# Performance work log

Hardware: AMD Instinct MI355X
Metric: run time of the kernel (lower is better)

## Reference

```python
import jax, jax.numpy as jnp
import numpy as np

B, T, C, H = 2, 2048, 1024, 16
D = C // H
THETA = 10000.0


def setup_inputs() -> dict:
    key = jax.random.key(0)
    k1, k2, k3 = jax.random.split(key, 3)
    x = jax.random.normal(k1, (B, T, C), dtype=jnp.float32)
    tok_mask = jnp.ones((B, T), dtype=bool)
    # torch Linear weights stored transposed: y = x @ W.T; we store [in, out]
    W_qkv = jax.random.normal(k2, (C, 3 * C), dtype=jnp.float32) / np.sqrt(C)
    W_o = jax.random.normal(k3, (C, C), dtype=jnp.float32) / np.sqrt(C)
    return {"x": x, "tok_mask": tok_mask, "W_qkv": W_qkv, "W_o": W_o}


def _rope_tables(t_len):
    # NOTE: source uses exponents arange(1, D+1, 2)/D and positions starting at 1
    exps = jnp.arange(1, D + 1, 2, dtype=jnp.float32)[: D // 2] / D
    w = 1.0 / (THETA ** exps)                      # [D/2]
    t = jnp.arange(1, t_len + 1, dtype=jnp.float32)  # [T]
    ang = t[:, None] * w[None, :]                  # [T, D/2]
    return jnp.sin(ang), jnp.cos(ang)


def _rope(x, sin, cos):
    # x: [B, H, T, D]; rotate interleaved pairs
    x1 = x[..., ::2]
    x2 = x[..., 1::2]
    r1 = x1 * cos - x2 * sin
    r2 = x1 * sin + x2 * cos
    return jnp.stack((r1, r2), axis=-1).reshape(x.shape)


def reference(x, tok_mask, W_qkv, W_o):
    b, t, c = x.shape
    qkv = x @ W_qkv                                   # [B,T,3C]
    q, k, v = jnp.split(qkv, 3, axis=-1)
    def heads(z):
        return z.reshape(b, t, H, D).transpose(0, 2, 1, 3)  # [B,H,T,D]
    q, k, v = heads(q), heads(k), heads(v)
    sin, cos = _rope_tables(t)
    q = _rope(q, sin, cos)
    k = _rope(k, sin, cos)
    scores = jnp.einsum('bhqd,bhkd->bhqk', q, k) / jnp.sqrt(jnp.float32(D))
    # mask[b,i,j] = tok_mask[b,i] & tok_mask[b,j] & causal
    mask = tok_mask[:, None, :, None] & tok_mask[:, None, None, :]  # [B,1,T,T]
    causal = jnp.tril(jnp.ones((t, t), dtype=bool))
    mask = mask & causal[None, None, :, :]
    scores = jnp.where(mask, scores, jnp.float32(-1e9))
    att = jax.nn.softmax(scores, axis=-1)             # dropout p=0 (eval)
    y = jnp.einsum('bhqk,bhkd->bhqd', att, v)
    y = y.transpose(0, 2, 1, 3).reshape(b, t, c)
    return y @ W_o
```

## Files before the change

### kernel.cpp

```cpp
#include <hip/hip_runtime.h>
#include <hip/hip_bf16.h>

typedef __bf16 bf16x8 __attribute__((ext_vector_type(8)));
typedef short s16x4 __attribute__((ext_vector_type(4)));
typedef float floatx4 __attribute__((ext_vector_type(4)));
typedef __hip_bfloat16 bf16;

#define T_SEQ 2048
#define NH 16
#define HD 64
#define CDIM 1024

__device__ __forceinline__ void gload16(const bf16* g, bf16* ldsbase) {
  __builtin_amdgcn_global_load_lds((const __attribute__((address_space(1))) void*)g,
                                   (__attribute__((address_space(3))) void*)ldsbase, 16, 0, 0);
}

__global__ __launch_bounds__(256) void cast_bf16_kernel(const float* __restrict__ in,
                                                        bf16* __restrict__ out) {
  int i = blockIdx.x * 256 + threadIdx.x;
  const float4 v = ((const float4*)in)[i];
  union { bf16 h[4]; uint2 u; } p;
  p.h[0] = __float2bfloat16(v.x);
  p.h[1] = __float2bfloat16(v.y);
  p.h[2] = __float2bfloat16(v.z);
  p.h[3] = __float2bfloat16(v.w);
  ((uint2*)out)[i] = p.u;
}

__global__ __launch_bounds__(256) void transpose_cast(const float* __restrict__ in,
                                                      bf16* __restrict__ out,
                                                      int R, int Cc) {
  __shared__ float tile[32][33];
  const int bx = blockIdx.x * 32;
  const int by = blockIdx.y * 32;
  const int tx = threadIdx.x & 31, ty = threadIdx.x >> 5;
#pragma unroll
  for (int i = 0; i < 32; i += 8)
    tile[ty + i][tx] = in[(size_t)(by + ty + i) * Cc + bx + tx];
  __syncthreads();
#pragma unroll
  for (int i = 0; i < 32; i += 8)
    out[(size_t)(bx + ty + i) * R + by + tx] = __float2bfloat16(tile[tx][ty + i]);
}

__global__ void rope_tab_kernel(float2* __restrict__ tab) {
  int idx = blockIdx.x * 256 + threadIdx.x;
  int t = idx >> 5, j = idx & 31;
  float w = exp2f(-13.287712379549449f * (float)(2 * j + 1) * (1.0f / 64.0f));
  float ang = (float)(t + 1) * w;
  tab[idx] = make_float2(cosf(ang), sinf(ang));
}

template <int MODE>
__global__ __launch_bounds__(256) void gemm_bt(
    const bf16* __restrict__ A, const bf16* __restrict__ BT, float* __restrict__ CoutF,
    const float2* __restrict__ tab, bf16* __restrict__ Qr, bf16* __restrict__ Kr,
    bf16* __restrict__ Vt, int M, int N, int K) {
  constexpr int LDK = 32;
  __shared__ __align__(16) bf16 As[128 * LDK];
  __shared__ __align__(16) bf16 Bs[128 * LDK];
  const int tid = threadIdx.x, lane = tid & 63, wave = tid >> 6;
  const int quad = lane >> 4, c16 = lane & 15;
  const int tile_m = blockIdx.y * 128, tile_n = blockIdx.x * 128;
  const int wm = (wave >> 1) * 64, wn = (wave & 1) * 64;
  const int r0 = tid >> 2, cp4 = tid & 3;
  bf16* ldsA0 = &As[wave * 512];
  bf16* ldsA1 = &As[2048 + wave * 512];
  bf16* ldsB0 = &Bs[wave * 512];
  bf16* ldsB1 = &Bs[2048 + wave * 512];
  floatx4 acc[4][4] = {};
  for (int k0 = 0; k0 < K; k0 += 32) {
    __syncthreads();
    gload16(&A[(size_t)(tile_m + r0) * K + k0 + cp4 * 8], ldsA0);
    gload16(&A[(size_t)(tile_m + r0 + 64) * K + k0 + cp4 * 8], ldsA1);
    gload16(&BT[(size_t)(tile_n + r0) * K + k0 + cp4 * 8], ldsB0);
    gload16(&BT[(size_t)(tile_n + r0 + 64) * K + k0 + cp4 * 8], ldsB1);
    __syncthreads();
    bf16x8 af[4], bfr[4];
#pragma unroll
    for (int i = 0; i < 4; i++)
      af[i] = *(const bf16x8*)&As[(wm + i * 16 + c16) * LDK + quad * 8];
#pragma unroll
    for (int i = 0; i < 4; i++)
      bfr[i] = *(const bf16x8*)&Bs[(wn + i * 16 + c16) * LDK + quad * 8];
#pragma unroll
    for (int mi = 0; mi < 4; mi++)
#pragma unroll
      for (int ni = 0; ni < 4; ni++)
        acc[mi][ni] = __builtin_amdgcn_mfma_f32_16x16x32_bf16(af[mi], bfr[ni], acc[mi][ni], 0, 0, 0);
  }
  if (MODE == 0) {
#pragma unroll
    for (int mi = 0; mi < 4; mi++) {
      int row0 = tile_m + wm + mi * 16 + quad * 4;
#pragma unroll
      for (int ni = 0; ni < 4; ni++) {
        int col = tile_n + wn + ni * 16 + c16;
#pragma unroll
        for (int r = 0; r < 4; r++)
          CoutF[(size_t)(row0 + r) * N + col] = acc[mi][ni][r];
      }
    }
  } else {
#pragma unroll
    for (int ni = 0; ni < 4; ni++) {
      int colg = tile_n + wn + ni * 16 + c16;
      int seg = colg >> 10;
      int cc = colg & 1023;
      int h = cc >> 6, d = cc & 63, j = d >> 1;
#pragma unroll
      for (int mi = 0; mi < 4; mi++) {
        int row0 = tile_m + wm + mi * 16 + quad * 4;
#pragma unroll
        for (int r = 0; r < 4; r++) {
          int rowg = row0 + r;
          int b = rowg >> 11, t = rowg & 2047;
          float val = acc[mi][ni][r];
          float partner = __shfl_xor(val, 1, 64);
          size_t bh = (size_t)(b * NH + h);
          if (seg == 2) {
            Vt[(bh * HD + d) * T_SEQ + t] = __float2bfloat16(val);
          } else {
            float2 sc = tab[t * 32 + j];
            float outv = ((d & 1) == 0) ? (val * sc.x - partner * sc.y)
                                        : (val * sc.x + partner * sc.y);
            bf16* dst = (seg == 0) ? Qr : Kr;
            dst[(bh * T_SEQ + t) * HD + d] = __float2bfloat16(outv);
          }
        }
      }
    }
  }
}

__global__ __launch_bounds__(256) void attn_kernel(const bf16* __restrict__ Qr,
                                                   const bf16* __restrict__ Kr,
                                                   const bf16* __restrict__ Vt,
                                                   bf16* __restrict__ Y) {
  constexpr int DPAD = 72;
  __shared__ __align__(16) bf16 Ks[64 * DPAD];
  __shared__ __align__(16) bf16 Vs[64 * DPAD];
  __shared__ __align__(16) bf16 Ps[4][16 * DPAD];
  const int qtile = 31 - (blockIdx.x >> 5), bh = blockIdx.x & 31;
  const int b = bh >> 4, h = bh & 15;
  const int tid = threadIdx.x, lane = tid & 63, wave = tid >> 6;
  const int quad = lane >> 4, c16 = lane & 15;
  const size_t hoff = (size_t)bh * T_SEQ * HD;
  const int row0 = tid >> 3, cp = tid & 7;
  const int qbase = qtile * 64;
  const int qg = qbase + wave * 16 + c16;
  bf16x8 qf0 = *(const bf16x8*)&Qr[hoff + (size_t)qg * HD + quad * 8];
  bf16x8 qf1 = *(const bf16x8*)&Qr[hoff + (size_t)qg * HD + 32 + quad * 8];
  floatx4 o_acc[4] = {};
  float m_run = -1e30f, l_run = 0.f;
  bf16x8 kreg0 = *(const bf16x8*)&Kr[hoff + (size_t)row0 * HD + cp * 8];
  bf16x8 kreg1 = *(const bf16x8*)&Kr[hoff + (size_t)(row0 + 32) * HD + cp * 8];
  bf16x8 vreg0 = *(const bf16x8*)&Vt[hoff + (size_t)row0 * T_SEQ + cp * 8];
  bf16x8 vreg1 = *(const bf16x8*)&Vt[hoff + (size_t)(row0 + 32) * T_SEQ + cp * 8];
  for (int kt = 0; kt <= qtile; ++kt) {
    const int kbase = kt * 64;
    __syncthreads();
    *(bf16x8*)&Ks[row0 * DPAD + cp * 8] = kreg0;
    *(bf16x8*)&Ks[(row0 + 32) * DPAD + cp * 8] = kreg1;
    *(bf16x8*)&Vs[row0 * DPAD + cp * 8] = vreg0;
    *(bf16x8*)&Vs[(row0 + 32) * DPAD + cp * 8] = vreg1;
    __syncthreads();
    if (kt < qtile) {
      const int nb = kbase + 64;
      kreg0 = *(const bf16x8*)&Kr[hoff + (size_t)(nb + row0) * HD + cp * 8];
      kreg1 = *(const bf16x8*)&Kr[hoff + (size_t)(nb + row0 + 32) * HD + cp * 8];
      vreg0 = *(const bf16x8*)&Vt[hoff + (size_t)row0 * T_SEQ + nb + cp * 8];
      vreg1 = *(const bf16x8*)&Vt[hoff + (size_t)(row0 + 32) * T_SEQ + nb + cp * 8];
    }
    floatx4 s[4];
#pragma unroll
    for (int nt = 0; nt < 4; nt++) {
      bf16x8 kf0 = *(const bf16x8*)&Ks[(nt * 16 + c16) * DPAD + quad * 8];
      bf16x8 kf1 = *(const bf16x8*)&Ks[(nt * 16 + c16) * DPAD + 32 + quad * 8];
      floatx4 z = {0.f, 0.f, 0.f, 0.f};
      z = __builtin_amdgcn_mfma_f32_16x16x32_bf16(kf0, qf0, z, 0, 0, 0);
      z = __builtin_amdgcn_mfma_f32_16x16x32_bf16(kf1, qf1, z, 0, 0, 0);
      s[nt] = z;
    }
    const bool diag = (kt == qtile);
    float mloc = -1e30f;
#pragma unroll
    for (int nt = 0; nt < 4; nt++)
#pragma unroll
      for (int r = 0; r < 4; r++) {
        float v = s[nt][r] * 0.125f;
        if (diag) {
          int kg = kbase + nt * 16 + quad * 4 + r;
          v = (kg <= qg) ? v : -1e30f;
        }
        s[nt][r] = v;
        mloc = fmaxf(mloc, v);
      }
    mloc = fmaxf(mloc, __shfl_xor(mloc, 16, 64));
    mloc = fmaxf(mloc, __shfl_xor(mloc, 32, 64));
    float mn = fmaxf(m_run, mloc);
    float alpha = __expf(m_run - mn);
    m_run = mn;
    float lloc = 0.f;
    union { bf16 h[4]; s16x4 sv; } ph[4];
#pragma unroll
    for (int nt = 0; nt < 4; nt++)
#pragma unroll
      for (int r = 0; r < 4; r++) {
        float pp = __expf(s[nt][r] - mn);
        lloc += pp;
        ph[nt].h[r] = __float2bfloat16(pp);
      }
    lloc += __shfl_xor(lloc, 16, 64);
    lloc += __shfl_xor(lloc, 32, 64);
    l_run = l_run * alpha + lloc;
#pragma unroll
    for (int nt = 0; nt < 4; nt++)
      *(s16x4*)&Ps[wave][c16 * DPAD + nt * 16 + quad * 4] = ph[nt].sv;
    float a_bc[4];
#pragma unroll
    for (int r = 0; r < 4; r++) a_bc[r] = __shfl(alpha, quad * 4 + r, 16);
#pragma unroll
    for (int dt = 0; dt < 4; dt++)
#pragma unroll
      for (int r = 0; r < 4; r++) o_acc[dt][r] *= a_bc[r];
    bf16x8 pf0 = *(const bf16x8*)&Ps[wave][c16 * DPAD + quad * 8];
    bf16x8 pf1 = *(const bf16x8*)&Ps[wave][c16 * DPAD + 32 + quad * 8];
#pragma unroll
    for (int dt = 0; dt < 4; dt++) {
      bf16x8 vf0 = *(const bf16x8*)&Vs[(dt * 16 + c16) * DPAD + quad * 8];
      bf16x8 vf1 = *(const bf16x8*)&Vs[(dt * 16 + c16) * DPAD + 32 + quad * 8];
      o_acc[dt] = __builtin_amdgcn_mfma_f32_16x16x32_bf16(pf0, vf0, o_acc[dt], 0, 0, 0);
      o_acc[dt] = __builtin_amdgcn_mfma_f32_16x16x32_bf16(pf1, vf1, o_acc[dt], 0, 0, 0);
    }
  }
  float linv = 1.0f / l_run;
  float l_bc[4];
#pragma unroll
  for (int r = 0; r < 4; r++) l_bc[r] = __shfl(linv, quad * 4 + r, 16);
#pragma unroll
  for (int dt = 0; dt < 4; dt++)
#pragma unroll
    for (int r = 0; r < 4; r++) {
      int t = qbase + wave * 16 + quad * 4 + r;
      Y[((size_t)(b * T_SEQ + t)) * CDIM + h * HD + dt * 16 + c16] =
          __float2bfloat16(o_acc[dt][r] * l_bc[r]);
    }
}

extern "C" void kernel_launch(void* const* d_in, const int* in_sizes, int n_in,
                              void* d_out, int out_size, void* d_ws, size_t ws_size,
                              hipStream_t stream) {
  const float* x    = (const float*)d_in[0];
  const float* Wqkv = (const float*)d_in[2];
  const float* Wo   = (const float*)d_in[3];
  float* out = (float*)d_out;

  bf16* ws    = (bf16*)d_ws;
  bf16* Xb    = ws;
  bf16* WqkvT = Xb + 4194304;
  bf16* WoT   = WqkvT + 3072 * 1024;
  bf16* Qr    = WoT + 1024 * 1024;
  bf16* Kr    = Qr + 4194304;
  bf16* Vt    = Kr + 4194304;
  bf16* Y     = Vt + 4194304;
  float2* tab = (float2*)(Y + 4194304);

  cast_bf16_kernel<<<4194304 / (256 * 4), 256, 0, stream>>>(x, Xb);
  transpose_cast<<<dim3(3072 / 32, 1024 / 32), 256, 0, stream>>>(Wqkv, WqkvT, 1024, 3072);
  transpose_cast<<<dim3(1024 / 32, 1024 / 32), 256, 0, stream>>>(Wo, WoT, 1024, 1024);
  rope_tab_kernel<<<65536 / 256, 256, 0, stream>>>(tab);
  gemm_bt<1><<<dim3(3072 / 128, 4096 / 128), 256, 0, stream>>>(
      Xb, WqkvT, nullptr, tab, Qr, Kr, Vt, 4096, 3072, 1024);
  attn_kernel<<<dim3(1024), 256, 0, stream>>>(Qr, Kr, Vt, Y);
  gemm_bt<0><<<dim3(1024 / 128, 4096 / 128), 256, 0, stream>>>(
      Y, WoT, out, nullptr, nullptr, nullptr, nullptr, 4096, 1024, 1024);
}
```

Baseline: 214.1 us.

## Double-buffer attention K/V tiles, swizzle GEMM LDS, fuse prep kernels

The attention kernel now keeps two LDS buffers for K and V. The next tile is written into the alternate buffer after the current tile's MFMAs, so each iteration needs one barrier instead of two. The GEMM applies an XOR swizzle to the 16-byte chunk position in LDS to reduce bank conflicts on fragment reads. The four preprocessing launches (cast, two transposes, rope table) are merged into one kernel indexed by block id, which removes launch overhead. Attention padding drops from 72 to 68 bf16 per row. That leaves 16-byte vector LDS accesses misaligned on odd rows, which may split them or raise conflicts, and the second K/V buffer adds LDS use that could lower occupancy.

```diff
diff --git a/kernel.cpp b/kernel.cpp
--- a/kernel.cpp
+++ b/kernel.cpp
@@ -16,40 +16,52 @@
                                    (__attribute__((address_space(3))) void*)ldsbase, 16, 0, 0);
 }
 
-__global__ __launch_bounds__(256) void cast_bf16_kernel(const float* __restrict__ in,
-                                                        bf16* __restrict__ out) {
-  int i = blockIdx.x * 256 + threadIdx.x;
-  const float4 v = ((const float4*)in)[i];
-  union { bf16 h[4]; uint2 u; } p;
-  p.h[0] = __float2bfloat16(v.x);
-  p.h[1] = __float2bfloat16(v.y);
-  p.h[2] = __float2bfloat16(v.z);
-  p.h[3] = __float2bfloat16(v.w);
-  ((uint2*)out)[i] = p.u;
-}
-
-__global__ __launch_bounds__(256) void transpose_cast(const float* __restrict__ in,
-                                                      bf16* __restrict__ out,
-                                                      int R, int Cc) {
+__global__ __launch_bounds__(256) void prep_kernel(const float* __restrict__ x,
+                                                   const float* __restrict__ Wqkv,
+                                                   const float* __restrict__ Wo,
+                                                   bf16* __restrict__ Xb,
+                                                   bf16* __restrict__ WqkvT,
+                                                   bf16* __restrict__ WoT,
+                                                   float2* __restrict__ tab) {
   __shared__ float tile[32][33];
-  const int bx = blockIdx.x * 32;
-  const int by = blockIdx.y * 32;
-  const int tx = threadIdx.x & 31, ty = threadIdx.x >> 5;
-#pragma unroll
-  for (int i = 0; i < 32; i += 8)
-    tile[ty + i][tx] = in[(size_t)(by + ty + i) * Cc + bx + tx];
-  __syncthreads();
-#pragma unroll
-  for (int i = 0; i < 32; i += 8)
-    out[(size_t)(bx + ty + i) * R + by + tx] = __float2bfloat16(tile[tx][ty + i]);
-}
-
-__global__ void rope_tab_kernel(float2* __restrict__ tab) {
-  int idx = blockIdx.x * 256 + threadIdx.x;
-  int t = idx >> 5, j = idx & 31;
-  float w = exp2f(-13.287712379549449f * (float)(2 * j + 1) * (1.0f / 64.0f));
-  float ang = (float)(t + 1) * w;
-  tab[idx] = make_float2(cosf(ang), sinf(ang));
+  const int bid = blockIdx.x, tid = threadIdx.x;
+  if (bid < 4096) {
+    int i = bid * 256 + tid;
+    const float4 v = ((const float4*)x)[i];
+    union { bf16 h[4]; uint2 u; } pk;
+    pk.h[0] = __float2bfloat16(v.x);
+    pk.h[1] = __float2bfloat16(v.y);
+    pk.h[2] = __float2bfloat16(v.z);
+    pk.h[3] = __float2bfloat16(v.w);
+    ((uint2*)Xb)[i] = pk.u;
+  } else if (bid < 8192) {
+    const float* in;
+    bf16* out;
+    int bx, by, R, Cc;
+    if (bid < 7168) {
+      int t = bid - 4096;
+      in = Wqkv; out = WqkvT; R = 1024; Cc = 3072;
+      bx = (t % 96) * 32; by = (t / 96) * 32;
+    } else {
+      int t = bid - 7168;
+      in = Wo; out = WoT; R = 1024; Cc = 1024;
+      bx = (t & 31) * 32; by = (t >> 5) * 32;
+    }
+    const int tx = tid & 31, ty = tid >> 5;
+#pragma unroll
+    for (int i = 0; i < 32; i += 8)
+      tile[ty + i][tx] = in[(size_t)(by + ty + i) * Cc + bx + tx];
+    __syncthreads();
+#pragma unroll
+    for (int i = 0; i < 32; i += 8)
+      out[(size_t)(bx + ty + i) * R + by + tx] = __float2bfloat16(tile[tx][ty + i]);
+  } else {
+    int idx = (bid - 8192) * 256 + tid;
+    int t = idx >> 5, j = idx & 31;
+    float w = exp2f(-13.287712379549449f * (float)(2 * j + 1) * (1.0f / 64.0f));
+    float ang = (float)(t + 1) * w;
+    tab[idx] = make_float2(cosf(ang), sinf(ang));
+  }
 }
 
 template <int MODE>
@@ -65,6 +77,8 @@
   const int tile_m = blockIdx.y * 128, tile_n = blockIdx.x * 128;
   const int wm = (wave >> 1) * 64, wn = (wave & 1) * 64;
   const int r0 = tid >> 2, cp4 = tid & 3;
+  const int csw = (cp4 ^ ((r0 >> 1) & 3)) * 8;
+  const int swr = (quad ^ ((c16 >> 1) & 3)) * 8;
   bf16* ldsA0 = &As[wave * 512];
   bf16* ldsA1 = &As[2048 + wave * 512];
   bf16* ldsB0 = &Bs[wave * 512];
@@ -72,18 +86,18 @@
   floatx4 acc[4][4] = {};
   for (int k0 = 0; k0 < K; k0 += 32) {
     __syncthreads();
-    gload16(&A[(size_t)(tile_m + r0) * K + k0 + cp4 * 8], ldsA0);
-    gload16(&A[(size_t)(tile_m + r0 + 64) * K + k0 + cp4 * 8], ldsA1);
-    gload16(&BT[(size_t)(tile_n + r0) * K + k0 + cp4 * 8], ldsB0);
-    gload16(&BT[(size_t)(tile_n + r0 + 64) * K + k0 + cp4 * 8], ldsB1);
+    gload16(&A[(size_t)(tile_m + r0) * K + k0 + csw], ldsA0);
+    gload16(&A[(size_t)(tile_m + r0 + 64) * K + k0 + csw], ldsA1);
+    gload16(&BT[(size_t)(tile_n + r0) * K + k0 + csw], ldsB0);
+    gload16(&BT[(size_t)(tile_n + r0 + 64) * K + k0 + csw], ldsB1);
     __syncthreads();
     bf16x8 af[4], bfr[4];
 #pragma unroll
     for (int i = 0; i < 4; i++)
-      af[i] = *(const bf16x8*)&As[(wm + i * 16 + c16) * LDK + quad * 8];
+      af[i] = *(const bf16x8*)&As[(wm + i * 16 + c16) * LDK + swr];
 #pragma unroll
     for (int i = 0; i < 4; i++)
-      bfr[i] = *(const bf16x8*)&Bs[(wn + i * 16 + c16) * LDK + quad * 8];
+      bfr[i] = *(const bf16x8*)&Bs[(wn + i * 16 + c16) * LDK + swr];
 #pragma unroll
     for (int mi = 0; mi < 4; mi++)
 #pragma unroll
@@ -138,9 +152,9 @@
                                                    const bf16* __restrict__ Kr,
                                                    const bf16* __restrict__ Vt,
                                                    bf16* __restrict__ Y) {
-  constexpr int DPAD = 72;
-  __shared__ __align__(16) bf16 Ks[64 * DPAD];
-  __shared__ __align__(16) bf16 Vs[64 * DPAD];
+  constexpr int DPAD = 68;
+  __shared__ __align__(16) bf16 Ks[2][64 * DPAD];
+  __shared__ __align__(16) bf16 Vs[2][64 * DPAD];
   __shared__ __align__(16) bf16 Ps[4][16 * DPAD];
   const int qtile = 31 - (blockIdx.x >> 5), bh = blockIdx.x & 31;
   const int b = bh >> 4, h = bh & 15;
@@ -158,14 +172,14 @@
   bf16x8 kreg1 = *(const bf16x8*)&Kr[hoff + (size_t)(row0 + 32) * HD + cp * 8];
   bf16x8 vreg0 = *(const bf16x8*)&Vt[hoff + (size_t)row0 * T_SEQ + cp * 8];
   bf16x8 vreg1 = *(const bf16x8*)&Vt[hoff + (size_t)(row0 + 32) * T_SEQ + cp * 8];
+  *(bf16x8*)&Ks[0][row0 * DPAD + cp * 8] = kreg0;
+  *(bf16x8*)&Ks[0][(row0 + 32) * DPAD + cp * 8] = kreg1;
+  *(bf16x8*)&Vs[0][row0 * DPAD + cp * 8] = vreg0;
+  *(bf16x8*)&Vs[0][(row0 + 32) * DPAD + cp * 8] = vreg1;
+  __syncthreads();
   for (int kt = 0; kt <= qtile; ++kt) {
     const int kbase = kt * 64;
-    __syncthreads();
-    *(bf16x8*)&Ks[row0 * DPAD + cp * 8] = kreg0;
-    *(bf16x8*)&Ks[(row0 + 32) * DPAD + cp * 8] = kreg1;
-    *(bf16x8*)&Vs[row0 * DPAD + cp * 8] = vreg0;
-    *(bf16x8*)&Vs[(row0 + 32) * DPAD + cp * 8] = vreg1;
-    __syncthreads();
+    const int cur = kt & 1;
     if (kt < qtile) {
       const int nb = kbase + 64;
       kreg0 = *(const bf16x8*)&Kr[hoff + (size_t)(nb + row0) * HD + cp * 8];
@@ -176,8 +190,8 @@
     floatx4 s[4];
 #pragma unroll
     for (int nt = 0; nt < 4; nt++) {
-      bf16x8 kf0 = *(const bf16x8*)&Ks[(nt * 16 + c16) * DPAD + quad * 8];
-      bf16x8 kf1 = *(const bf16x8*)&Ks[(nt * 16 + c16) * DPAD + 32 + quad * 8];
+      bf16x8 kf0 = *(const bf16x8*)&Ks[cur][(nt * 16 + c16) * DPAD + quad * 8];
+      bf16x8 kf1 = *(const bf16x8*)&Ks[cur][(nt * 16 + c16) * DPAD + 32 + quad * 8];
       floatx4 z = {0.f, 0.f, 0.f, 0.f};
       z = __builtin_amdgcn_mfma_f32_16x16x32_bf16(kf0, qf0, z, 0, 0, 0);
       z = __builtin_amdgcn_mfma_f32_16x16x32_bf16(kf1, qf1, z, 0, 0, 0);
@@ -229,11 +243,19 @@
     bf16x8 pf1 = *(const bf16x8*)&Ps[wave][c16 * DPAD + 32 + quad * 8];
 #pragma unroll
     for (int dt = 0; dt < 4; dt++) {
-      bf16x8 vf0 = *(const bf16x8*)&Vs[(dt * 16 + c16) * DPAD + quad * 8];
-      bf16x8 vf1 = *(const bf16x8*)&Vs[(dt * 16 + c16) * DPAD + 32 + quad * 8];
+      bf16x8 vf0 = *(const bf16x8*)&Vs[cur][(dt * 16 + c16) * DPAD + quad * 8];
+      bf16x8 vf1 = *(const bf16x8*)&Vs[cur][(dt * 16 + c16) * DPAD + 32 + quad * 8];
       o_acc[dt] = __builtin_amdgcn_mfma_f32_16x16x32_bf16(pf0, vf0, o_acc[dt], 0, 0, 0);
       o_acc[dt] = __builtin_amdgcn_mfma_f32_16x16x32_bf16(pf1, vf1, o_acc[dt], 0, 0, 0);
     }
+    if (kt < qtile) {
+      const int nxt = cur ^ 1;
+      *(bf16x8*)&Ks[nxt][row0 * DPAD + cp * 8] = kreg0;
+      *(bf16x8*)&Ks[nxt][(row0 + 32) * DPAD + cp * 8] = kreg1;
+      *(bf16x8*)&Vs[nxt][row0 * DPAD + cp * 8] = vreg0;
+      *(bf16x8*)&Vs[nxt][(row0 + 32) * DPAD + cp * 8] = vreg1;
+    }
+    __syncthreads();
   }
   float linv = 1.0f / l_run;
   float l_bc[4];
@@ -267,10 +289,7 @@
   bf16* Y     = Vt + 4194304;
   float2* tab = (float2*)(Y + 4194304);
 
-  cast_bf16_kernel<<<4194304 / (256 * 4), 256, 0, stream>>>(x, Xb);
-  transpose_cast<<<dim3(3072 / 32, 1024 / 32), 256, 0, stream>>>(Wqkv, WqkvT, 1024, 3072);
-  transpose_cast<<<dim3(1024 / 32, 1024 / 32), 256, 0, stream>>>(Wo, WoT, 1024, 1024);
-  rope_tab_kernel<<<65536 / 256, 256, 0, stream>>>(tab);
+  prep_kernel<<<dim3(8448), 256, 0, stream>>>(x, Wqkv, Wo, Xb, WqkvT, WoT, tab);
   gemm_bt<1><<<dim3(3072 / 128, 4096 / 128), 256, 0, stream>>>(
       Xb, WqkvT, nullptr, tab, Qr, Kr, Vt, 4096, 3072, 1024);
   attn_kernel<<<dim3(1024), 256, 0, stream>>>(Qr, Kr, Vt, Y);
```

Result: faster. 208.3 us (-2.7%).
